# Optimization experiments

Measured on AMD Instinct MI355X. Metric: run time of the kernel, lower is better.

The kernel has to match this reference:

```python
import jax, jax.numpy as jnp
import numpy as np

B, NL, NP, H, L, NRBF, TDIM = 16, 32, 192, 128, 4, 16, 64
CUTOFF = 4.0
N = NL + NP  # nodes per graph
MSG_IN = 3 * H + NRBF + 1  # 401
_STEP = CUTOFF / (NRBF - 1)
GAMMA = 1.0 / (_STEP * _STEP)
CENTERS = jnp.linspace(0.0, CUTOFF, NRBF, dtype=jnp.float32)


def _build_edges():
    # same topology for every graph; build template once, offset per graph
    lig = np.arange(NL)
    poc = np.arange(NL, N)
    lig_n = np.roll(lig, -1)
    poc_n = np.roll(poc, -1)
    pr = np.repeat(poc, NL)
    lr = np.tile(lig, NP)
    src = np.concatenate([lig, lig_n, poc, poc_n, pr, lr])
    dst = np.concatenate([lig_n, lig, poc_n, poc, lr, pr])
    et = np.concatenate([
        np.zeros(2 * NL, np.int64), np.ones(2 * NP, np.int64),
        np.full(NL * NP, 2, np.int64), np.full(NL * NP, 3, np.int64)])
    off = (np.arange(B) * N)[:, None]
    src = (src[None] + off).reshape(-1)
    dst = (dst[None] + off).reshape(-1)
    et = np.tile(et, B)
    return jnp.asarray(src, jnp.int32), jnp.asarray(dst, jnp.int32), jnp.asarray(et, jnp.int32)


def _cycle_pe(n):
    pos = jnp.arange(n, dtype=jnp.float32)
    ang = 2.0 * jnp.pi * pos / max(float(n), 1.0)
    return jnp.stack([jnp.sin(ang), jnp.cos(ang)], axis=-1)  # [n, 2]


def _ln(x, g, b):
    m = x.mean(-1, keepdims=True)
    v = ((x - m) ** 2).mean(-1, keepdims=True)
    return (x - m) / jnp.sqrt(v + 1e-5) * g + b


def _smean(vals, idx, n):
    s = jax.ops.segment_sum(vals, idx, num_segments=n)
    c = jax.ops.segment_sum(jnp.ones(vals.shape[0], vals.dtype), idx, num_segments=n)
    return s / jnp.clip(c, 1.0)[:, None]


def _sin_emb(t):
    half = TDIM // 2
    f = jnp.exp(-jnp.log(10000.0) / (half - 1) * jnp.arange(half, dtype=jnp.float32))
    a = t[:, None] * f[None, :]
    return jnp.concatenate([jnp.sin(a), jnp.cos(a)], axis=-1)  # [B, TDIM]


def setup_inputs() -> dict:
    key = jax.random.key(0)
    ks = iter(jax.random.split(key, 48))
    rn = lambda shape, s=0.05: jax.random.normal(next(ks), shape, jnp.float32) * s
    return dict(
        ligand_coords=jax.random.normal(next(ks), (B, NL, 2), jnp.float32),
        pocket_coords=jax.random.normal(next(ks), (B, NP, 2), jnp.float32),
        t=jax.random.uniform(next(ks), (B,), jnp.float32) * 1000.0,
        w_in=rn((4, H)), b_in=jnp.zeros((H,), jnp.float32),
        node_emb=rn((2, H)),
        ln_in_g=jnp.ones((H,), jnp.float32), ln_in_b=jnp.zeros((H,), jnp.float32),
        time_w1=rn((TDIM, H)), time_b1=jnp.zeros((H,), jnp.float32),
        time_w2=rn((H, H)), time_b2=jnp.zeros((H,), jnp.float32),
        edge_emb=rn((L, 4, H)),
        msg_w1=rn((L, MSG_IN, H)), msg_b1=jnp.zeros((L, H), jnp.float32),
        msg_w2=rn((L, H, H)), msg_b2=jnp.zeros((L, H), jnp.float32),
        upd_w1=rn((L, 2 * H, H)), upd_b1=jnp.zeros((L, H), jnp.float32),
        upd_w2=rn((L, H, H)), upd_b2=jnp.zeros((L, H), jnp.float32),
        ln_g=jnp.ones((L, H), jnp.float32), ln_b=jnp.zeros((L, H), jnp.float32),
        head_w1=rn((H, H)), head_b1=jnp.zeros((H,), jnp.float32),
        head_w2=rn((H, 1)), head_b2=jnp.zeros((1,), jnp.float32),
    )


def _forward(ligand_coords, pocket_coords, t, w_in, b_in, node_emb, ln_in_g, ln_in_b,
             time_w1, time_b1, time_w2, time_b2, edge_emb, msg_w1, msg_b1, msg_w2, msg_b2,
             upd_w1, upd_b1, upd_w2, upd_b2, ln_g, ln_b,
             head_w1, head_b1, head_w2, head_b2, src, dst, etype):
    coords = jnp.concatenate([ligand_coords, pocket_coords], axis=1)  # [B, N, 2]
    cyc = jnp.concatenate([_cycle_pe(NL), _cycle_pe(NP)], axis=0)  # [N, 2]
    feats = jnp.concatenate([coords, jnp.broadcast_to(cyc[None], (B, N, 2))], axis=-1)
    feats = feats.reshape(B * N, 4)
    coords_flat = coords.reshape(B * N, 2)
    node_type = jnp.tile(jnp.concatenate([jnp.ones(NL, jnp.int32), jnp.zeros(NP, jnp.int32)]), B)

    h = feats @ w_in + b_in + node_emb[node_type]
    te = _sin_emb(t) @ time_w1 + time_b1
    te = jax.nn.silu(te) @ time_w2 + time_b2  # [B, H]
    h = (h.reshape(B, N, H) + te[:, None, :]).reshape(B * N, H)
    h = _ln(h, ln_in_g, ln_in_b)

    rel = coords_flat[src] - coords_flat[dst]
    dist = jnp.linalg.norm(rel, axis=-1)  # [E]
    radial = jnp.exp(-GAMMA * (dist[:, None] - CENTERS[None, :]) ** 2)  # [E, NRBF]

    for l in range(L):
        ef = edge_emb[l][etype]  # [E, H]
        msg_in = jnp.concatenate([h[src], h[dst], ef, radial, dist[:, None]], axis=-1)
        m = jax.nn.silu(msg_in @ msg_w1[l] + msg_b1[l])
        m = jax.nn.silu(m @ msg_w2[l] + msg_b2[l])
        agg = _smean(m, dst, B * N)
        u = jax.nn.silu(jnp.concatenate([h, agg], axis=-1) @ upd_w1[l] + upd_b1[l])
        u = u @ upd_w2[l] + upd_b2[l]
        h = _ln(h + u, ln_g[l], ln_b[l])

    # ligand nodes are the first NL nodes of each graph; equal count per graph
    pooled = h.reshape(B, N, H)[:, :NL, :].mean(axis=1)  # [B, H]
    out = jax.nn.silu(pooled @ head_w1 + head_b1) @ head_w2 + head_b2
    return out[:, 0]


def reference(ligand_coords, pocket_coords, t, w_in, b_in, node_emb, ln_in_g, ln_in_b,
              time_w1, time_b1, time_w2, time_b2, edge_emb, msg_w1, msg_b1, msg_w2, msg_b2,
              upd_w1, upd_b1, upd_w2, upd_b2, ln_g, ln_b,
              head_w1, head_b1, head_w2, head_b2):
    src, dst, etype = _build_edges()
    return _forward(ligand_coords, pocket_coords, t, w_in, b_in, node_emb, ln_in_g, ln_in_b,
                    time_w1, time_b1, time_w2, time_b2, edge_emb, msg_w1, msg_b1, msg_w2, msg_b2,
                    upd_w1, upd_b1, upd_w2, upd_b2, ln_g, ln_b,
                    head_w1, head_b1, head_w2, head_b2, src, dst, etype)
```

## Files before the change

### kernel.cpp

```cpp
#include <hip/hip_runtime.h>
#include <math.h>

#define NBATCH 16
#define NLIG   32
#define NPOC   192
#define NNODE  224
#define TOTN   (NBATCH*NNODE)
#define HD     128
#define NLAYER 4
#define NRBF   16
#define TDIMC  64
#define EBI2   (NBATCH*NLIG*NPOC)
#define NTILE  ((2*EBI2)/128)
#define NPBP   4
#define NPBU   4
#define GAMMA_C 14.0625f
#define RSTEP   0.26666666666666666f
#define TWOPI   6.283185307179586f
#define LDH    136
#define RADH   40

typedef _Float16 half_t;
typedef __attribute__((ext_vector_type(8))) _Float16 half8;
typedef __attribute__((ext_vector_type(4))) _Float16 half4;
typedef __attribute__((ext_vector_type(4))) float f32x4;

__device__ __forceinline__ float silu_f(float x) { return x / (1.0f + __expf(-x)); }

__global__ void k_time(const float* __restrict__ t,
                       const float* __restrict__ w1, const float* __restrict__ b1,
                       const float* __restrict__ w2, const float* __restrict__ b2,
                       float* __restrict__ te) {
  __shared__ float emb[TDIMC];
  __shared__ float mid[HD];
  const int b = blockIdx.x, j = threadIdx.x;
  if (j < TDIMC) {
    const int half = TDIMC / 2;
    const float tv = t[b];
    const int i = j & 31;
    const float f = __expf(-logf(10000.0f) / (float)(half - 1) * (float)i);
    const float a = tv * f;
    emb[j] = (j < half) ? sinf(a) : cosf(a);
  }
  __syncthreads();
  float acc = b1[j];
  for (int k = 0; k < TDIMC; ++k) acc += emb[k] * w1[k*HD + j];
  mid[j] = silu_f(acc);
  __syncthreads();
  float acc2 = b2[j];
  for (int k = 0; k < HD; ++k) acc2 += mid[k] * w2[k*HD + j];
  te[b*HD + j] = acc2;
}

__global__ void k_init(const float* __restrict__ ligc, const float* __restrict__ pocc,
                       const float* __restrict__ w_in, const float* __restrict__ b_in,
                       const float* __restrict__ nemb, const float* __restrict__ te,
                       const float* __restrict__ lng, const float* __restrict__ lnb,
                       float* __restrict__ h) {
  const int n = blockIdx.x, j = threadIdx.x;
  const int g = n / NNODE, loc = n - g*NNODE;
  const bool isl = loc < NLIG;
  float cx, cy, ang;
  if (isl) { cx = ligc[(g*NLIG + loc)*2]; cy = ligc[(g*NLIG + loc)*2 + 1];
             ang = TWOPI * (float)loc / 32.0f; }
  else { const int lp = loc - NLIG;
         cx = pocc[(g*NPOC + lp)*2]; cy = pocc[(g*NPOC + lp)*2 + 1];
         ang = TWOPI * (float)lp / 192.0f; }
  const float sa = sinf(ang), ca = cosf(ang);
  const int ty = isl ? 1 : 0;
  const float v = b_in[j] + cx*w_in[j] + cy*w_in[HD + j] + sa*w_in[2*HD + j]
                + ca*w_in[3*HD + j] + nemb[ty*HD + j] + te[g*HD + j];
  __shared__ float sm[2], sq[2];
  float s = v, q = v*v;
  #pragma unroll
  for (int o = 32; o > 0; o >>= 1) { s += __shfl_down(s, o); q += __shfl_down(q, o); }
  if ((j & 63) == 0) { sm[j >> 6] = s; sq[j >> 6] = q; }
  __syncthreads();
  const float mean = (sm[0] + sm[1]) * (1.0f/HD);
  const float var  = (sq[0] + sq[1]) * (1.0f/HD) - mean*mean;
  h[n*HD + j] = (v - mean) * rsqrtf(var + 1e-5f) * lng[j] + lnb[j];
}

__global__ void k_w2cvt(const float* __restrict__ mw2, const float* __restrict__ mw1,
                        half_t* __restrict__ w2h, half_t* __restrict__ wrbfh) {
  if (blockIdx.x >= 8) {
    const int l = blockIdx.x - 8;
    const float* W1 = mw1 + (size_t)l * 401 * HD;
    const int t = threadIdx.x;
    const int j = t & 127, k0 = (t >> 7) * 16;
    half_t* out = wrbfh + (size_t)l*HD*32 + (size_t)j*32 + k0;
    for (int k = k0; k < k0 + 16; ++k) {
      float v = 0.f;
      if (k < 16) v = W1[(384 + k)*HD + j];
      else if (k == 16) v = W1[400*HD + j];
      out[k - k0] = (half_t)v;
    }
    return;
  }
  __shared__ float ft[64][129];
  const int l = blockIdx.x >> 1, k0 = (blockIdx.x & 1) * 64;
  const float* W2 = mw2 + (size_t)l*HD*HD;
  const int t = threadIdx.x;
  for (int i = 0; i < 32; ++i) {
    const int idx = t + i*256;
    const int k = idx >> 7, j = idx & 127;
    ft[k][j] = W2[(k0 + k)*HD + j];
  }
  __syncthreads();
  half_t* out = w2h + (size_t)l*HD*HD;
  for (int i = 0; i < 32; ++i) {
    const int idx = t + i*256;
    const int j = idx >> 6, k = idx & 63;
    out[j*HD + k0 + k] = (half_t)ft[k][j];
  }
}

__global__ void k_project(const float* __restrict__ h, const float* __restrict__ mw1,
                          const float* __restrict__ mb1, const float* __restrict__ eemb,
                          float* __restrict__ hs, float* __restrict__ hd,
                          float* __restrict__ agg, float* __restrict__ eb, int l) {
  const int j = threadIdx.x;
  const float* W1 = mw1 + (size_t)l * 401 * HD;
  if (blockIdx.x == TOTN / NPBP) {
    for (int et = 0; et < 4; ++et) {
      const float* ef = eemb + ((size_t)l * 4 + et) * HD;
      float acc = mb1[l*HD + j];
      for (int k = 0; k < HD; ++k) acc += ef[k] * W1[(256 + k)*HD + j];
      eb[et*HD + j] = acc;
    }
    return;
  }
  __shared__ float hr[NPBP][HD];
  const int n0 = blockIdx.x * NPBP;
  #pragma unroll
  for (int nn = 0; nn < NPBP; ++nn) hr[nn][j] = h[(n0 + nn)*HD + j];
  __syncthreads();
  float as[NPBP], ad[NPBP];
  #pragma unroll
  for (int nn = 0; nn < NPBP; ++nn) { as[nn] = 0.f; ad[nn] = 0.f; }
  for (int k = 0; k < HD; ++k) {
    const float ws = W1[k*HD + j];
    const float wd = W1[(128 + k)*HD + j];
    #pragma unroll
    for (int nn = 0; nn < NPBP; ++nn) { as[nn] += hr[nn][k]*ws; ad[nn] += hr[nn][k]*wd; }
  }
  #pragma unroll
  for (int nn = 0; nn < NPBP; ++nn) {
    hs[(n0 + nn)*HD + j]  = as[nn];
    hd[(n0 + nn)*HD + j]  = ad[nn];
    agg[(n0 + nn)*HD + j] = 0.f;
  }
}

__global__ __launch_bounds__(256, 3)
void k_edges(const float* __restrict__ ligc, const float* __restrict__ pocc,
             const float* __restrict__ hs, const float* __restrict__ hd,
             const half_t* __restrict__ wrbfh, const float* __restrict__ mb2,
             const half_t* __restrict__ w2h, const float* __restrict__ eb,
             float* __restrict__ agg, int l) {
  extern __shared__ char lds_raw[];
  half_t* m_t   = (half_t*)lds_raw;
  half_t* rad_h = m_t + 128*LDH;
  float*  b2l   = (float*)(rad_h + 128*RADH);

  const int tid = threadIdx.x;
  const int bid = blockIdx.x;
  const int et  = (bid < NTILE/2) ? 2 : 3;

  if (tid < 128) {
    b2l[tid] = mb2[l*HD + tid];
    const int e = tid;
    int g, sl, dl;
    if (et == 2) {
      const int idx = bid*128 + e;
      g = idx / 6144; const int r0 = idx - g*6144;
      const int i = r0 / 192; const int p = r0 - i*192;
      sl = NLIG + p; dl = i;
    } else {
      const int idx = bid*128 + e - EBI2;
      g = idx / 6144; const int r0 = idx - g*6144;
      const int p = r0 >> 5; const int i = r0 & 31;
      sl = i; dl = NLIG + p;
    }
    float sx, sy, dx, dy;
    if (sl < NLIG) { sx = ligc[(g*NLIG + sl)*2]; sy = ligc[(g*NLIG + sl)*2 + 1]; }
    else { const int lp = sl - NLIG; sx = pocc[(g*NPOC + lp)*2]; sy = pocc[(g*NPOC + lp)*2 + 1]; }
    if (dl < NLIG) { dx = ligc[(g*NLIG + dl)*2]; dy = ligc[(g*NLIG + dl)*2 + 1]; }
    else { const int lp = dl - NLIG; dx = pocc[(g*NPOC + lp)*2]; dy = pocc[(g*NPOC + lp)*2 + 1]; }
    const float rx = sx - dx, ry = sy - dy;
    const float d = sqrtf(rx*rx + ry*ry);
    half_t* rp = rad_h + e*RADH;
    #pragma unroll
    for (int rr = 0; rr < NRBF; ++rr) {
      const float u = d - RSTEP * (float)rr;
      rp[rr] = (half_t)__expf(-GAMMA_C * u * u);
    }
    rp[16] = (half_t)d;
    #pragma unroll
    for (int k = 17; k < 32; ++k) rp[k] = (half_t)0.f;
  }
  __syncthreads();

  {
    const int lane = tid & 63;
    const int q = lane >> 4, c15 = lane & 15;
    const int ebase = (tid >> 6) * 32;
    const half_t* WR = wrbfh + (size_t)l*HD*32;
    half8 af[8];
    #pragma unroll
    for (int jb = 0; jb < 8; ++jb)
      af[jb] = *(const half8*)&WR[(size_t)(jb*16 + c15)*32 + 8*q];
    #pragma unroll
    for (int eb2 = 0; eb2 < 2; ++eb2) {
      const half8 bf2 = *(const half8*)&rad_h[(ebase + eb2*16 + c15)*RADH + 8*q];
      const int e = ebase + eb2*16 + c15;
      #pragma unroll
      for (int jb = 0; jb < 8; ++jb) {
        f32x4 a2 = (f32x4){0.f, 0.f, 0.f, 0.f};
        a2 = __builtin_amdgcn_mfma_f32_16x16x32_f16(af[jb], bf2, a2, 0, 0, 0);
        half4 hv;
        hv[0] = (half_t)a2[0]; hv[1] = (half_t)a2[1];
        hv[2] = (half_t)a2[2]; hv[3] = (half_t)a2[3];
        *(half4*)&m_t[(size_t)e*LDH + jb*16 + q*4] = hv;
      }
    }
  }
  __syncthreads();

  {
    const int j = tid & 127, eh = tid >> 7;
    const int e0 = eh * 64;
    const float ebv = eb[et*HD + j];

    if (et == 2) {
      const int idx0 = bid*128 + e0;
      const int g = idx0 / 6144; const int r0 = idx0 - g*6144;
      const int i = r0 / 192;    const int p0 = r0 - i*192;
      const int gn = g*NNODE;
      const float hdc = hd[(size_t)(gn + i)*HD + j] + ebv;
      const float* hp = hs + (size_t)(gn + NLIG + p0)*HD + j;
      #pragma unroll 8
      for (int v = 0; v < 64; ++v) {
        const int e = e0 + v;
        const float pre = (float)m_t[e*LDH + j] + hp[(size_t)v*HD] + hdc;
        m_t[e*LDH + j] = (half_t)silu_f(pre);
      }
    } else {
      const int idx0 = bid*128 + e0 - EBI2;
      const int g = idx0 / 6144; const int r0 = idx0 - g*6144;
      const int p0 = r0 >> 5;
      const int gn = g*NNODE;
      const float* hsp = hs + (size_t)gn*HD + j;
      float hsr[32];
      #pragma unroll
      for (int ii = 0; ii < 32; ++ii) hsr[ii] = hsp[(size_t)ii*HD];
      #pragma unroll
      for (int hf = 0; hf < 2; ++hf) {
        const float hdc = hd[(size_t)(gn + NLIG + p0 + hf)*HD + j] + ebv;
        #pragma unroll 8
        for (int ii = 0; ii < 32; ++ii) {
          const int e = e0 + hf*32 + ii;
          const float pre = (float)m_t[e*LDH + j] + hsr[ii] + hdc;
          m_t[e*LDH + j] = (half_t)silu_f(pre);
        }
      }
    }
  }
  __syncthreads();

  {
    const int wv = tid >> 6, lane = tid & 63;
    const int q = lane >> 4, c15 = lane & 15;
    const int ebase = wv*32;
    int dst;
    if (et == 2) {
      const int idx = bid*128 + ebase;
      const int g = idx / 6144; const int r0 = idx - g*6144;
      dst = g*NNODE + r0/192;
    } else {
      const int idx = bid*128 + ebase - EBI2;
      const int g = idx / 6144; const int r0 = idx - g*6144;
      dst = g*NNODE + NLIG + (r0 >> 5);
    }
    const half_t* W2H = w2h + (size_t)l*HD*HD;
    f32x4 acc[2][8];
    #pragma unroll
    for (int ii = 0; ii < 2; ++ii)
      #pragma unroll
      for (int jj = 0; jj < 8; ++jj) acc[ii][jj] = (f32x4){0.f,0.f,0.f,0.f};
    for (int k0 = 0; k0 < HD; k0 += 32) {
      half8 af[2], bf[8];
      #pragma unroll
      for (int ii = 0; ii < 2; ++ii)
        af[ii] = *(const half8*)&m_t[(ebase + ii*16 + c15)*LDH + k0 + 8*q];
      #pragma unroll
      for (int jj = 0; jj < 8; ++jj)
        bf[jj] = *(const half8*)&W2H[(size_t)(jj*16 + c15)*HD + k0 + 8*q];
      #pragma unroll
      for (int ii = 0; ii < 2; ++ii)
        #pragma unroll
        for (int jj = 0; jj < 8; ++jj)
          acc[ii][jj] = __builtin_amdgcn_mfma_f32_16x16x32_f16(af[ii], bf[jj], acc[ii][jj], 0, 0, 0);
    }
    #pragma unroll
    for (int jj = 0; jj < 8; ++jj) {
      const int col = jj*16 + c15;
      const float bb = b2l[col];
      float s = 0.f;
      #pragma unroll
      for (int ii = 0; ii < 2; ++ii) {
        s += silu_f(acc[ii][jj][0] + bb) + silu_f(acc[ii][jj][1] + bb)
           + silu_f(acc[ii][jj][2] + bb) + silu_f(acc[ii][jj][3] + bb);
      }
      s += __shfl_xor(s, 16);
      s += __shfl_xor(s, 32);
      if (q == 0) atomicAdd(&agg[(size_t)dst*HD + col], s);
    }
  }
}

__global__ void k_update(const float* __restrict__ ligc, const float* __restrict__ pocc,
                         const float* __restrict__ hs, const float* __restrict__ hd,
                         const float* __restrict__ mw1, const float* __restrict__ mb2,
                         const float* __restrict__ mw2, const float* __restrict__ eb,
                         const float* __restrict__ agg,
                         const float* __restrict__ uw1, const float* __restrict__ ub1,
                         const float* __restrict__ uw2, const float* __restrict__ ub2,
                         const float* __restrict__ lng, const float* __restrict__ lnb,
                         float* __restrict__ h, int l) {
  const int j = threadIdx.x;
  const int n0 = blockIdx.x * NPBU;
  __shared__ float wrbf[NRBF*HD];
  __shared__ float wdst[HD], ebs[2*HD], b2s[HD];
  __shared__ float mA[NPBU][HD], mB[NPBU][HD], hr[NPBU][HD], ar[NPBU][HD], ur[NPBU][HD];
  __shared__ float radS[NPBU][2][NRBF];
  __shared__ float distS[NPBU][2];
  __shared__ float sm[2][NPBU], sq[2][NPBU];
  const float* W1 = mw1 + (size_t)l * 401 * HD;
  const float* W2 = mw2 + (size_t)l * HD * HD;
  for (int idx = j; idx < NRBF*HD; idx += HD) wrbf[idx] = W1[384*HD + idx];
  wdst[j]     = W1[400*HD + j];
  ebs[j]      = eb[j];
  ebs[HD + j] = eb[HD + j];
  b2s[j]      = mb2[l*HD + j];
  {
    const int nn = j >> 5, rr = j & 31;
    if (rr < 16) {
      const int n = n0 + nn;
      const int g = n / NNODE, loc = n - g*NNODE;
      const bool isl = loc < NLIG;
      float nx, ny;
      if (isl) { nx = ligc[(g*NLIG + loc)*2]; ny = ligc[(g*NLIG + loc)*2 + 1]; }
      else { const int lp = loc - NLIG; nx = pocc[(g*NPOC + lp)*2]; ny = pocc[(g*NPOC + lp)*2 + 1]; }
      #pragma unroll
      for (int ab = 0; ab < 2; ++ab) {
        int sl;
        if (isl) sl = (ab == 0) ? ((loc + NLIG - 1) & 31) : ((loc + 1) & 31);
        else { const int lp = loc - NLIG;
               const int sp = (ab == 0) ? (lp + NPOC - 1) % NPOC : (lp + 1) % NPOC;
               sl = NLIG + sp; }
        float sx, sy;
        if (sl < NLIG) { sx = ligc[(g*NLIG + sl)*2]; sy = ligc[(g*NLIG + sl)*2 + 1]; }
        else { const int lp = sl - NLIG; sx = pocc[(g*NPOC + lp)*2]; sy = pocc[(g*NPOC + lp)*2 + 1]; }
        const float rx = sx - nx, ry = sy - ny;
        const float d = sqrtf(rx*rx + ry*ry);
        const float u = d - RSTEP * (float)rr;
        radS[nn][ab][rr] = __expf(-GAMMA_C * u * u);
        if (rr == 0) distS[nn][ab] = d;
      }
    }
  }
  __syncthreads();
  for (int nn = 0; nn < NPBU; ++nn) {
    const int n = n0 + nn;
    const int g = n / NNODE, loc = n - g*NNODE;
    const bool isl = loc < NLIG;
    int slA, slB, etc_;
    if (isl) { slA = (loc + NLIG - 1) & 31; slB = (loc + 1) & 31; etc_ = 0; }
    else { const int lp = loc - NLIG;
           slA = NLIG + (lp + NPOC - 1) % NPOC; slB = NLIG + (lp + 1) % NPOC; etc_ = 1; }
    const int snA = g*NNODE + slA, snB = g*NNODE + slB;
    const float base = hd[n*HD + j] + ebs[etc_*HD + j];
    float pA = hs[snA*HD + j] + base + distS[nn][0]*wdst[j];
    float pB = hs[snB*HD + j] + base + distS[nn][1]*wdst[j];
    #pragma unroll
    for (int rr = 0; rr < NRBF; ++rr) {
      const float w = wrbf[rr*HD + j];
      pA += radS[nn][0][rr] * w;
      pB += radS[nn][1][rr] * w;
    }
    mA[nn][j] = silu_f(pA);
    mB[nn][j] = silu_f(pB);
    hr[nn][j] = h[n*HD + j];
  }
  __syncthreads();
  {
    float aA[NPBU], aB[NPBU];
    #pragma unroll
    for (int nn = 0; nn < NPBU; ++nn) { aA[nn] = 0.f; aB[nn] = 0.f; }
    for (int k = 0; k < HD; ++k) {
      const float w = W2[k*HD + j];
      #pragma unroll
      for (int nn = 0; nn < NPBU; ++nn) { aA[nn] += mA[nn][k]*w; aB[nn] += mB[nn][k]*w; }
    }
    #pragma unroll
    for (int nn = 0; nn < NPBU; ++nn) {
      const int n = n0 + nn;
      const int loc = n % NNODE;
      const float inv_deg = (loc < NLIG) ? (1.0f/194.0f) : (1.0f/34.0f);
      const float cyc = silu_f(aA[nn] + b2s[j]) + silu_f(aB[nn] + b2s[j]);
      ar[nn][j] = (agg[n*HD + j] + cyc) * inv_deg;
    }
  }
  __syncthreads();
  {
    float aU[NPBU];
    #pragma unroll
    for (int nn = 0; nn < NPBU; ++nn) aU[nn] = 0.f;
    const float* U1 = uw1 + (size_t)l * 2 * HD * HD;
    for (int k = 0; k < HD; ++k) {
      const float w = U1[k*HD + j];
      #pragma unroll
      for (int nn = 0; nn < NPBU; ++nn) aU[nn] += hr[nn][k]*w;
    }
    for (int k = 0; k < HD; ++k) {
      const float w = U1[(HD + k)*HD + j];
      #pragma unroll
      for (int nn = 0; nn < NPBU; ++nn) aU[nn] += ar[nn][k]*w;
    }
    const float b1v = ub1[l*HD + j];
    #pragma unroll
    for (int nn = 0; nn < NPBU; ++nn) ur[nn][j] = silu_f(aU[nn] + b1v);
  }
  __syncthreads();
  {
    float aV[NPBU];
    #pragma unroll
    for (int nn = 0; nn < NPBU; ++nn) aV[nn] = 0.f;
    const float* U2 = uw2 + (size_t)l * HD * HD;
    for (int k = 0; k < HD; ++k) {
      const float w = U2[k*HD + j];
      #pragma unroll
      for (int nn = 0; nn < NPBU; ++nn) aV[nn] += ur[nn][k]*w;
    }
    const float b2v = ub2[l*HD + j];
    const float gv = lng[l*HD + j], bv = lnb[l*HD + j];
    float xs[NPBU];
    #pragma unroll
    for (int nn = 0; nn < NPBU; ++nn) {
      xs[nn] = hr[nn][j] + aV[nn] + b2v;
      float s = xs[nn], q = xs[nn]*xs[nn];
      #pragma unroll
      for (int o = 32; o > 0; o >>= 1) { s += __shfl_down(s, o); q += __shfl_down(q, o); }
      if ((j & 63) == 0) { sm[j >> 6][nn] = s; sq[j >> 6][nn] = q; }
    }
    __syncthreads();
    #pragma unroll
    for (int nn = 0; nn < NPBU; ++nn) {
      const float mean = (sm[0][nn] + sm[1][nn]) * (1.0f/HD);
      const float var  = (sq[0][nn] + sq[1][nn]) * (1.0f/HD) - mean*mean;
      h[(n0 + nn)*HD + j] = (xs[nn] - mean) * rsqrtf(var + 1e-5f) * gv + bv;
    }
  }
}

__global__ void k_head(const float* __restrict__ h, const float* __restrict__ hw1,
                       const float* __restrict__ hb1, const float* __restrict__ hw2,
                       const float* __restrict__ hb2, float* __restrict__ out) {
  const int b = blockIdx.x, j = threadIdx.x;
  __shared__ float pool[HD], mid[HD];
  __shared__ float sm[2];
  float s = 0.f;
  #pragma unroll
  for (int i = 0; i < NLIG; ++i) s += h[(b*NNODE + i)*HD + j];
  pool[j] = s * (1.0f/NLIG);
  __syncthreads();
  float acc = hb1[j];
  for (int k = 0; k < HD; ++k) acc += pool[k] * hw1[k*HD + j];
  mid[j] = silu_f(acc);
  __syncthreads();
  float v = mid[j] * hw2[j];
  #pragma unroll
  for (int o = 32; o > 0; o >>= 1) v += __shfl_down(v, o);
  if ((j & 63) == 0) sm[j >> 6] = v;
  __syncthreads();
  if (j == 0) out[b] = sm[0] + sm[1] + hb2[0];
}

extern "C" void kernel_launch(void* const* d_in, const int* in_sizes, int n_in,
                              void* d_out, int out_size, void* d_ws, size_t ws_size,
                              hipStream_t stream) {
  (void)in_sizes; (void)n_in; (void)out_size; (void)ws_size;
  const float* ligc = (const float*)d_in[0];
  const float* pocc = (const float*)d_in[1];
  const float* tarr = (const float*)d_in[2];
  const float* w_in = (const float*)d_in[3];
  const float* b_in = (const float*)d_in[4];
  const float* nemb = (const float*)d_in[5];
  const float* lnig = (const float*)d_in[6];
  const float* lnib = (const float*)d_in[7];
  const float* tw1  = (const float*)d_in[8];
  const float* tb1  = (const float*)d_in[9];
  const float* tw2  = (const float*)d_in[10];
  const float* tb2  = (const float*)d_in[11];
  const float* eemb = (const float*)d_in[12];
  const float* mw1  = (const float*)d_in[13];
  const float* mb1  = (const float*)d_in[14];
  const float* mw2  = (const float*)d_in[15];
  const float* mb2  = (const float*)d_in[16];
  const float* uw1  = (const float*)d_in[17];
  const float* ub1  = (const float*)d_in[18];
  const float* uw2  = (const float*)d_in[19];
  const float* ub2  = (const float*)d_in[20];
  const float* lng  = (const float*)d_in[21];
  const float* lnb  = (const float*)d_in[22];
  const float* hw1  = (const float*)d_in[23];
  const float* hb1  = (const float*)d_in[24];
  const float* hw2  = (const float*)d_in[25];
  const float* hb2  = (const float*)d_in[26];
  float* outp = (float*)d_out;

  float* ws  = (float*)d_ws;
  float* te  = ws;
  float* h   = te  + NBATCH*HD;
  float* hs  = h   + TOTN*HD;
  float* hd  = hs  + TOTN*HD;
  float* agg = hd  + TOTN*HD;
  float* eb  = agg + TOTN*HD;
  half_t* w2h   = (half_t*)(eb + 4*HD);
  half_t* wrbfh = w2h + (size_t)NLAYER*HD*HD;

  const int SMEM_EDGES = 128*LDH*2 + 128*RADH*2 + 128*4;
  hipFuncSetAttribute((const void*)k_edges, hipFuncAttributeMaxDynamicSharedMemorySize, SMEM_EDGES);

  k_time<<<NBATCH, HD, 0, stream>>>(tarr, tw1, tb1, tw2, tb2, te);
  k_init<<<TOTN, HD, 0, stream>>>(ligc, pocc, w_in, b_in, nemb, te, lnig, lnib, h);
  k_w2cvt<<<12, 256, 0, stream>>>(mw2, mw1, w2h, wrbfh);
  for (int l = 0; l < NLAYER; ++l) {
    k_project<<<TOTN/NPBP + 1, HD, 0, stream>>>(h, mw1, mb1, eemb, hs, hd, agg, eb, l);
    k_edges<<<NTILE, 256, SMEM_EDGES, stream>>>(ligc, pocc, hs, hd, wrbfh, mb2, w2h, eb, agg, l);
    k_update<<<TOTN/NPBU, HD, 0, stream>>>(ligc, pocc, hs, hd, mw1, mb2, mw2, eb, agg,
                                           uw1, ub1, uw2, ub2, lng, lnb, h, l);
  }
  k_head<<<NBATCH, HD, 0, stream>>>(h, hw1, hb1, hw2, hb2, outp);
}
```

Before: 508.2 us.

## Fuse message pre-activation into MFMA epilogue and next-layer projection into update

In the edge kernel, the hs/hd/edge-bias add and SiLU are applied straight on the MFMA accumulator registers. This removes a separate shared-memory pass and one barrier over the 128x128 message tile. The per-layer projection kernel is folded into the end of the update kernel, which now writes hs/hd for the next layer into ping-pong buffers and zeroes agg. All edge-type biases are precomputed once in the weight-convert kernel, and the update kernel runs with 256 threads, splitting each matvec across two halves. This cuts three kernel launches and a global round-trip per layer, at the cost of more shared memory and barriers in the update kernel and scattered global loads in the MFMA epilogue.

```diff
diff --git a/kernel.cpp b/kernel.cpp
--- a/kernel.cpp
+++ b/kernel.cpp
@@ -82,11 +82,25 @@
 }
 
 __global__ void k_w2cvt(const float* __restrict__ mw2, const float* __restrict__ mw1,
-                        half_t* __restrict__ w2h, half_t* __restrict__ wrbfh) {
+                        const float* __restrict__ mb1, const float* __restrict__ eemb,
+                        half_t* __restrict__ w2h, half_t* __restrict__ wrbfh,
+                        float* __restrict__ eb) {
+  const int t = threadIdx.x;
+  if (blockIdx.x >= 12) {
+    const int l = blockIdx.x - 12;
+    const float* W1 = mw1 + (size_t)l * 401 * HD;
+    const int j = t & 127, eth = t >> 7;
+    for (int et = eth; et < 4; et += 2) {
+      const float* ef = eemb + ((size_t)l * 4 + et) * HD;
+      float acc = mb1[l*HD + j];
+      for (int k = 0; k < HD; ++k) acc += ef[k] * W1[(256 + k)*HD + j];
+      eb[(l*4 + et)*HD + j] = acc;
+    }
+    return;
+  }
   if (blockIdx.x >= 8) {
     const int l = blockIdx.x - 8;
     const float* W1 = mw1 + (size_t)l * 401 * HD;
-    const int t = threadIdx.x;
     const int j = t & 127, k0 = (t >> 7) * 16;
     half_t* out = wrbfh + (size_t)l*HD*32 + (size_t)j*32 + k0;
     for (int k = k0; k < k0 + 16; ++k) {
@@ -100,7 +114,6 @@
   __shared__ float ft[64][129];
   const int l = blockIdx.x >> 1, k0 = (blockIdx.x & 1) * 64;
   const float* W2 = mw2 + (size_t)l*HD*HD;
-  const int t = threadIdx.x;
   for (int i = 0; i < 32; ++i) {
     const int idx = t + i*256;
     const int k = idx >> 7, j = idx & 127;
@@ -116,20 +129,10 @@
 }
 
 __global__ void k_project(const float* __restrict__ h, const float* __restrict__ mw1,
-                          const float* __restrict__ mb1, const float* __restrict__ eemb,
                           float* __restrict__ hs, float* __restrict__ hd,
-                          float* __restrict__ agg, float* __restrict__ eb, int l) {
+                          float* __restrict__ agg) {
   const int j = threadIdx.x;
-  const float* W1 = mw1 + (size_t)l * 401 * HD;
-  if (blockIdx.x == TOTN / NPBP) {
-    for (int et = 0; et < 4; ++et) {
-      const float* ef = eemb + ((size_t)l * 4 + et) * HD;
-      float acc = mb1[l*HD + j];
-      for (int k = 0; k < HD; ++k) acc += ef[k] * W1[(256 + k)*HD + j];
-      eb[et*HD + j] = acc;
-    }
-    return;
-  }
+  const float* W1 = mw1;
   __shared__ float hr[NPBP][HD];
   const int n0 = blockIdx.x * NPBP;
   #pragma unroll
@@ -205,65 +208,54 @@
     const int lane = tid & 63;
     const int q = lane >> 4, c15 = lane & 15;
     const int ebase = (tid >> 6) * 32;
+    int srcA, srcB, dst;
+    if (et == 2) {
+      const int idxA = bid*128 + ebase + c15;
+      const int g = idxA / 6144; const int r0 = idxA - g*6144;
+      const int i = r0 / 192, p = r0 - i*192;
+      dst  = g*NNODE + i;
+      srcA = g*NNODE + NLIG + p;
+      srcB = srcA + 16;
+    } else {
+      const int idxA = bid*128 + ebase + c15 - EBI2;
+      const int g = idxA / 6144; const int r0 = idxA - g*6144;
+      const int p = r0 >> 5, i = r0 & 31;
+      dst  = g*NNODE + NLIG + p;
+      srcA = g*NNODE + i;
+      srcB = g*NNODE + ((i + 16) & 31);
+    }
+    const float* hdrow = hd + (size_t)dst*HD;
+    const float* ebrow = eb + (size_t)(l*4 + et)*HD;
+    const float* hsA   = hs + (size_t)srcA*HD;
+    const float* hsB   = hs + (size_t)srcB*HD;
     const half_t* WR = wrbfh + (size_t)l*HD*32;
     half8 af[8];
     #pragma unroll
     for (int jb = 0; jb < 8; ++jb)
       af[jb] = *(const half8*)&WR[(size_t)(jb*16 + c15)*32 + 8*q];
-    #pragma unroll
-    for (int eb2 = 0; eb2 < 2; ++eb2) {
-      const half8 bf2 = *(const half8*)&rad_h[(ebase + eb2*16 + c15)*RADH + 8*q];
-      const int e = ebase + eb2*16 + c15;
-      #pragma unroll
-      for (int jb = 0; jb < 8; ++jb) {
-        f32x4 a2 = (f32x4){0.f, 0.f, 0.f, 0.f};
-        a2 = __builtin_amdgcn_mfma_f32_16x16x32_f16(af[jb], bf2, a2, 0, 0, 0);
-        half4 hv;
-        hv[0] = (half_t)a2[0]; hv[1] = (half_t)a2[1];
-        hv[2] = (half_t)a2[2]; hv[3] = (half_t)a2[3];
-        *(half4*)&m_t[(size_t)e*LDH + jb*16 + q*4] = hv;
+    const half8 bfA = *(const half8*)&rad_h[(ebase + c15)*RADH + 8*q];
+    const half8 bfB = *(const half8*)&rad_h[(ebase + 16 + c15)*RADH + 8*q];
+    const int eA = ebase + c15, eB = ebase + 16 + c15;
+    #pragma unroll
+    for (int jb = 0; jb < 8; ++jb) {
+      const int j0 = jb*16 + q*4;
+      f32x4 hde = *(const f32x4*)&hdrow[j0];
+      const f32x4 ebv = *(const f32x4*)&ebrow[j0];
+      #pragma unroll
+      for (int r = 0; r < 4; ++r) hde[r] += ebv[r];
+      f32x4 zero = (f32x4){0.f,0.f,0.f,0.f};
+      f32x4 aA = __builtin_amdgcn_mfma_f32_16x16x32_f16(af[jb], bfA, zero, 0, 0, 0);
+      f32x4 aB = __builtin_amdgcn_mfma_f32_16x16x32_f16(af[jb], bfB, zero, 0, 0, 0);
+      const f32x4 ha = *(const f32x4*)&hsA[j0];
+      const f32x4 hb = *(const f32x4*)&hsB[j0];
+      half4 hvA, hvB;
+      #pragma unroll
+      for (int r = 0; r < 4; ++r) {
+        hvA[r] = (half_t)silu_f(aA[r] + ha[r] + hde[r]);
+        hvB[r] = (half_t)silu_f(aB[r] + hb[r] + hde[r]);
       }
-    }
-  }
-  __syncthreads();
-
-  {
-    const int j = tid & 127, eh = tid >> 7;
-    const int e0 = eh * 64;
-    const float ebv = eb[et*HD + j];
-
-    if (et == 2) {
-      const int idx0 = bid*128 + e0;
-      const int g = idx0 / 6144; const int r0 = idx0 - g*6144;
-      const int i = r0 / 192;    const int p0 = r0 - i*192;
-      const int gn = g*NNODE;
-      const float hdc = hd[(size_t)(gn + i)*HD + j] + ebv;
-      const float* hp = hs + (size_t)(gn + NLIG + p0)*HD + j;
-      #pragma unroll 8
-      for (int v = 0; v < 64; ++v) {
-        const int e = e0 + v;
-        const float pre = (float)m_t[e*LDH + j] + hp[(size_t)v*HD] + hdc;
-        m_t[e*LDH + j] = (half_t)silu_f(pre);
-      }
-    } else {
-      const int idx0 = bid*128 + e0 - EBI2;
-      const int g = idx0 / 6144; const int r0 = idx0 - g*6144;
-      const int p0 = r0 >> 5;
-      const int gn = g*NNODE;
-      const float* hsp = hs + (size_t)gn*HD + j;
-      float hsr[32];
-      #pragma unroll
-      for (int ii = 0; ii < 32; ++ii) hsr[ii] = hsp[(size_t)ii*HD];
-      #pragma unroll
-      for (int hf = 0; hf < 2; ++hf) {
-        const float hdc = hd[(size_t)(gn + NLIG + p0 + hf)*HD + j] + ebv;
-        #pragma unroll 8
-        for (int ii = 0; ii < 32; ++ii) {
-          const int e = e0 + hf*32 + ii;
-          const float pre = (float)m_t[e*LDH + j] + hsr[ii] + hdc;
-          m_t[e*LDH + j] = (half_t)silu_f(pre);
-        }
-      }
+      *(half4*)&m_t[(size_t)eA*LDH + j0] = hvA;
+      *(half4*)&m_t[(size_t)eB*LDH + j0] = hvB;
     }
   }
   __syncthreads();
@@ -319,32 +311,40 @@
   }
 }
 
-__global__ void k_update(const float* __restrict__ ligc, const float* __restrict__ pocc,
-                         const float* __restrict__ hs, const float* __restrict__ hd,
-                         const float* __restrict__ mw1, const float* __restrict__ mb2,
-                         const float* __restrict__ mw2, const float* __restrict__ eb,
-                         const float* __restrict__ agg,
-                         const float* __restrict__ uw1, const float* __restrict__ ub1,
-                         const float* __restrict__ uw2, const float* __restrict__ ub2,
-                         const float* __restrict__ lng, const float* __restrict__ lnb,
-                         float* __restrict__ h, int l) {
-  const int j = threadIdx.x;
+__global__ __launch_bounds__(256, 4)
+void k_update(const float* __restrict__ ligc, const float* __restrict__ pocc,
+              const float* __restrict__ hs, const float* __restrict__ hd,
+              const float* __restrict__ mw1, const float* __restrict__ mb2,
+              const float* __restrict__ mw2, const float* __restrict__ eb,
+              float* __restrict__ agg,
+              const float* __restrict__ uw1, const float* __restrict__ ub1,
+              const float* __restrict__ uw2, const float* __restrict__ ub2,
+              const float* __restrict__ lng, const float* __restrict__ lnb,
+              float* __restrict__ h, float* __restrict__ hsn, float* __restrict__ hdn,
+              int l) {
+  const int tid = threadIdx.x;
+  const int j = tid & 127, hf = tid >> 7;
   const int n0 = blockIdx.x * NPBU;
   __shared__ float wrbf[NRBF*HD];
   __shared__ float wdst[HD], ebs[2*HD], b2s[HD];
-  __shared__ float mA[NPBU][HD], mB[NPBU][HD], hr[NPBU][HD], ar[NPBU][HD], ur[NPBU][HD];
+  __shared__ float mAB[2][NPBU][HD];
+  __shared__ float hr[NPBU][HD], ar[NPBU][HD], ur[NPBU][HD], ag[NPBU][HD], hnew[NPBU][HD];
+  __shared__ float pP[2][NPBU][HD];
   __shared__ float radS[NPBU][2][NRBF];
   __shared__ float distS[NPBU][2];
   __shared__ float sm[2][NPBU], sq[2][NPBU];
   const float* W1 = mw1 + (size_t)l * 401 * HD;
   const float* W2 = mw2 + (size_t)l * HD * HD;
-  for (int idx = j; idx < NRBF*HD; idx += HD) wrbf[idx] = W1[384*HD + idx];
-  wdst[j]     = W1[400*HD + j];
-  ebs[j]      = eb[j];
-  ebs[HD + j] = eb[HD + j];
-  b2s[j]      = mb2[l*HD + j];
-  {
-    const int nn = j >> 5, rr = j & 31;
+  for (int idx = tid; idx < NRBF*HD; idx += 256) wrbf[idx] = W1[384*HD + idx];
+  if (hf == 0) {
+    wdst[j] = W1[400*HD + j];
+    b2s[j]  = mb2[l*HD + j];
+  } else {
+    ebs[j]      = eb[(l*4 + 0)*HD + j];
+    ebs[HD + j] = eb[(l*4 + 1)*HD + j];
+  }
+  if (tid < 128) {
+    const int nn = tid >> 5, rr = tid & 31;
     if (rr < 16) {
       const int n = n0 + nn;
       const int g = n / NNODE, loc = n - g*NNODE;
@@ -371,95 +371,124 @@
     }
   }
   __syncthreads();
+  #pragma unroll
   for (int nn = 0; nn < NPBU; ++nn) {
     const int n = n0 + nn;
     const int g = n / NNODE, loc = n - g*NNODE;
     const bool isl = loc < NLIG;
-    int slA, slB, etc_;
-    if (isl) { slA = (loc + NLIG - 1) & 31; slB = (loc + 1) & 31; etc_ = 0; }
+    int sl, etc_;
+    if (isl) { sl = (hf == 0) ? ((loc + NLIG - 1) & 31) : ((loc + 1) & 31); etc_ = 0; }
     else { const int lp = loc - NLIG;
-           slA = NLIG + (lp + NPOC - 1) % NPOC; slB = NLIG + (lp + 1) % NPOC; etc_ = 1; }
-    const int snA = g*NNODE + slA, snB = g*NNODE + slB;
-    const float base = hd[n*HD + j] + ebs[etc_*HD + j];
-    float pA = hs[snA*HD + j] + base + distS[nn][0]*wdst[j];
-    float pB = hs[snB*HD + j] + base + distS[nn][1]*wdst[j];
-    #pragma unroll
-    for (int rr = 0; rr < NRBF; ++rr) {
-      const float w = wrbf[rr*HD + j];
-      pA += radS[nn][0][rr] * w;
-      pB += radS[nn][1][rr] * w;
-    }
-    mA[nn][j] = silu_f(pA);
-    mB[nn][j] = silu_f(pB);
-    hr[nn][j] = h[n*HD + j];
-  }
-  __syncthreads();
-  {
-    float aA[NPBU], aB[NPBU];
-    #pragma unroll
-    for (int nn = 0; nn < NPBU; ++nn) { aA[nn] = 0.f; aB[nn] = 0.f; }
+           sl = NLIG + ((hf == 0) ? (lp + NPOC - 1) % NPOC : (lp + 1) % NPOC); etc_ = 1; }
+    const int sn = g*NNODE + sl;
+    const float base = hd[(size_t)n*HD + j] + ebs[etc_*HD + j];
+    float p = hs[(size_t)sn*HD + j] + base + distS[nn][hf]*wdst[j];
+    #pragma unroll
+    for (int rr = 0; rr < NRBF; ++rr) p += radS[nn][hf][rr] * wrbf[rr*HD + j];
+    mAB[hf][nn][j] = silu_f(p);
+    if (hf == 0) hr[nn][j] = h[(size_t)n*HD + j];
+    else         ag[nn][j] = agg[(size_t)n*HD + j];
+  }
+  __syncthreads();
+  {
+    float a[NPBU];
+    #pragma unroll
+    for (int nn = 0; nn < NPBU; ++nn) a[nn] = 0.f;
     for (int k = 0; k < HD; ++k) {
       const float w = W2[k*HD + j];
       #pragma unroll
-      for (int nn = 0; nn < NPBU; ++nn) { aA[nn] += mA[nn][k]*w; aB[nn] += mB[nn][k]*w; }
-    }
-    #pragma unroll
-    for (int nn = 0; nn < NPBU; ++nn) {
-      const int n = n0 + nn;
-      const int loc = n % NNODE;
+      for (int nn = 0; nn < NPBU; ++nn) a[nn] += mAB[hf][nn][k]*w;
+    }
+    #pragma unroll
+    for (int nn = 0; nn < NPBU; ++nn) pP[hf][nn][j] = a[nn];
+  }
+  __syncthreads();
+  {
+    const float b = b2s[j];
+    for (int nn = hf*2; nn < hf*2 + 2; ++nn) {
+      const int loc = (n0 + nn) % NNODE;
       const float inv_deg = (loc < NLIG) ? (1.0f/194.0f) : (1.0f/34.0f);
-      const float cyc = silu_f(aA[nn] + b2s[j]) + silu_f(aB[nn] + b2s[j]);
-      ar[nn][j] = (agg[n*HD + j] + cyc) * inv_deg;
-    }
-  }
-  __syncthreads();
-  {
-    float aU[NPBU];
-    #pragma unroll
-    for (int nn = 0; nn < NPBU; ++nn) aU[nn] = 0.f;
-    const float* U1 = uw1 + (size_t)l * 2 * HD * HD;
+      ar[nn][j] = (ag[nn][j] + silu_f(pP[0][nn][j] + b) + silu_f(pP[1][nn][j] + b)) * inv_deg;
+    }
+  }
+  __syncthreads();
+  {
+    const float* U1 = uw1 + (size_t)l*2*HD*HD + (size_t)hf*HD*HD;
+    const float (*src)[HD] = (hf == 0) ? hr : ar;
+    float a[NPBU];
+    #pragma unroll
+    for (int nn = 0; nn < NPBU; ++nn) a[nn] = 0.f;
     for (int k = 0; k < HD; ++k) {
       const float w = U1[k*HD + j];
       #pragma unroll
-      for (int nn = 0; nn < NPBU; ++nn) aU[nn] += hr[nn][k]*w;
-    }
+      for (int nn = 0; nn < NPBU; ++nn) a[nn] += src[nn][k]*w;
+    }
+    #pragma unroll
+    for (int nn = 0; nn < NPBU; ++nn) pP[hf][nn][j] = a[nn];
+  }
+  __syncthreads();
+  {
+    const float b1v = ub1[l*HD + j];
+    for (int nn = hf*2; nn < hf*2 + 2; ++nn)
+      ur[nn][j] = silu_f(pP[0][nn][j] + pP[1][nn][j] + b1v);
+  }
+  __syncthreads();
+  {
+    const float* U2 = uw2 + (size_t)l*HD*HD;
+    float a[NPBU];
+    #pragma unroll
+    for (int nn = 0; nn < NPBU; ++nn) a[nn] = 0.f;
+    const int kb = hf*64;
+    for (int k = kb; k < kb + 64; ++k) {
+      const float w = U2[k*HD + j];
+      #pragma unroll
+      for (int nn = 0; nn < NPBU; ++nn) a[nn] += ur[nn][k]*w;
+    }
+    #pragma unroll
+    for (int nn = 0; nn < NPBU; ++nn) pP[hf][nn][j] = a[nn];
+  }
+  __syncthreads();
+  {
+    const float b2v = ub2[l*HD + j];
+    float xs[NPBU];
+    #pragma unroll
+    for (int nn = 0; nn < NPBU; ++nn) {
+      xs[nn] = hr[nn][j] + pP[0][nn][j] + pP[1][nn][j] + b2v;
+      float s = xs[nn], qq = xs[nn]*xs[nn];
+      #pragma unroll
+      for (int o = 32; o > 0; o >>= 1) { s += __shfl_down(s, o); qq += __shfl_down(qq, o); }
+      if (((j & 63) == 0) && hf == 0) { sm[j >> 6][nn] = s; sq[j >> 6][nn] = qq; }
+    }
+    __syncthreads();
+    if (hf == 0) {
+      const float gv = lng[l*HD + j], bv = lnb[l*HD + j];
+      #pragma unroll
+      for (int nn = 0; nn < NPBU; ++nn) {
+        const float mean = (sm[0][nn] + sm[1][nn]) * (1.0f/HD);
+        const float var  = (sq[0][nn] + sq[1][nn]) * (1.0f/HD) - mean*mean;
+        const float v = (xs[nn] - mean) * rsqrtf(var + 1e-5f) * gv + bv;
+        h[(size_t)(n0 + nn)*HD + j] = v;
+        hnew[nn][j] = v;
+      }
+    }
+  }
+  __syncthreads();
+  if (l < 3) {
+    const float* W1n = mw1 + (size_t)(l+1)*401*HD + (size_t)(hf ? 128 : 0)*HD;
+    float a[NPBU];
+    #pragma unroll
+    for (int nn = 0; nn < NPBU; ++nn) a[nn] = 0.f;
     for (int k = 0; k < HD; ++k) {
-      const float w = U1[(HD + k)*HD + j];
-      #pragma unroll
-      for (int nn = 0; nn < NPBU; ++nn) aU[nn] += ar[nn][k]*w;
-    }
-    const float b1v = ub1[l*HD + j];
-    #pragma unroll
-    for (int nn = 0; nn < NPBU; ++nn) ur[nn][j] = silu_f(aU[nn] + b1v);
-  }
-  __syncthreads();
-  {
-    float aV[NPBU];
-    #pragma unroll
-    for (int nn = 0; nn < NPBU; ++nn) aV[nn] = 0.f;
-    const float* U2 = uw2 + (size_t)l * HD * HD;
-    for (int k = 0; k < HD; ++k) {
-      const float w = U2[k*HD + j];
-      #pragma unroll
-      for (int nn = 0; nn < NPBU; ++nn) aV[nn] += ur[nn][k]*w;
-    }
-    const float b2v = ub2[l*HD + j];
-    const float gv = lng[l*HD + j], bv = lnb[l*HD + j];
-    float xs[NPBU];
-    #pragma unroll
-    for (int nn = 0; nn < NPBU; ++nn) {
-      xs[nn] = hr[nn][j] + aV[nn] + b2v;
-      float s = xs[nn], q = xs[nn]*xs[nn];
-      #pragma unroll
-      for (int o = 32; o > 0; o >>= 1) { s += __shfl_down(s, o); q += __shfl_down(q, o); }
-      if ((j & 63) == 0) { sm[j >> 6][nn] = s; sq[j >> 6][nn] = q; }
-    }
-    __syncthreads();
-    #pragma unroll
-    for (int nn = 0; nn < NPBU; ++nn) {
-      const float mean = (sm[0][nn] + sm[1][nn]) * (1.0f/HD);
-      const float var  = (sq[0][nn] + sq[1][nn]) * (1.0f/HD) - mean*mean;
-      h[(n0 + nn)*HD + j] = (xs[nn] - mean) * rsqrtf(var + 1e-5f) * gv + bv;
+      const float w = W1n[k*HD + j];
+      #pragma unroll
+      for (int nn = 0; nn < NPBU; ++nn) a[nn] += hnew[nn][k]*w;
+    }
+    float* outp = (hf == 0) ? hsn : hdn;
+    #pragma unroll
+    for (int nn = 0; nn < NPBU; ++nn) outp[(size_t)(n0 + nn)*HD + j] = a[nn];
+    if (hf == 0) {
+      #pragma unroll
+      for (int nn = 0; nn < NPBU; ++nn) agg[(size_t)(n0 + nn)*HD + j] = 0.f;
     }
   }
 }
@@ -523,24 +552,32 @@
   float* ws  = (float*)d_ws;
   float* te  = ws;
   float* h   = te  + NBATCH*HD;
-  float* hs  = h   + TOTN*HD;
-  float* hd  = hs  + TOTN*HD;
-  float* agg = hd  + TOTN*HD;
+  float* hs0 = h   + TOTN*HD;
+  float* hd0 = hs0 + TOTN*HD;
+  float* hs1 = hd0 + TOTN*HD;
+  float* hd1 = hs1 + TOTN*HD;
+  float* agg = hd1 + TOTN*HD;
   float* eb  = agg + TOTN*HD;
-  half_t* w2h   = (half_t*)(eb + 4*HD);
+  half_t* w2h   = (half_t*)(eb + 16*HD);
   half_t* wrbfh = w2h + (size_t)NLAYER*HD*HD;
+
+  float* hsb[2] = {hs0, hs1};
+  float* hdb[2] = {hd0, hd1};
 
   const int SMEM_EDGES = 128*LDH*2 + 128*RADH*2 + 128*4;
   hipFuncSetAttribute((const void*)k_edges, hipFuncAttributeMaxDynamicSharedMemorySize, SMEM_EDGES);
 
   k_time<<<NBATCH, HD, 0, stream>>>(tarr, tw1, tb1, tw2, tb2, te);
   k_init<<<TOTN, HD, 0, stream>>>(ligc, pocc, w_in, b_in, nemb, te, lnig, lnib, h);
-  k_w2cvt<<<12, 256, 0, stream>>>(mw2, mw1, w2h, wrbfh);
+  k_w2cvt<<<16, 256, 0, stream>>>(mw2, mw1, mb1, eemb, w2h, wrbfh, eb);
+  k_project<<<TOTN/NPBP, HD, 0, stream>>>(h, mw1, hs0, hd0, agg);
   for (int l = 0; l < NLAYER; ++l) {
-    k_project<<<TOTN/NPBP + 1, HD, 0, stream>>>(h, mw1, mb1, eemb, hs, hd, agg, eb, l);
-    k_edges<<<NTILE, 256, SMEM_EDGES, stream>>>(ligc, pocc, hs, hd, wrbfh, mb2, w2h, eb, agg, l);
-    k_update<<<TOTN/NPBU, HD, 0, stream>>>(ligc, pocc, hs, hd, mw1, mb2, mw2, eb, agg,
-                                           uw1, ub1, uw2, ub2, lng, lnb, h, l);
+    const int cur = l & 1, nxt = cur ^ 1;
+    k_edges<<<NTILE, 256, SMEM_EDGES, stream>>>(ligc, pocc, hsb[cur], hdb[cur],
+                                                wrbfh, mb2, w2h, eb, agg, l);
+    k_update<<<TOTN/NPBU, 256, 0, stream>>>(ligc, pocc, hsb[cur], hdb[cur], mw1, mb2, mw2,
+                                            eb, agg, uw1, ub1, uw2, ub2, lng, lnb,
+                                            h, hsb[nxt], hdb[nxt], l);
   }
   k_head<<<NBATCH, HD, 0, stream>>>(h, hw1, hb1, hw2, hb2, outp);
 }
```

Result: faster. 452.0 us (-11.0%).
